# Kernel optimization log

Hardware: AMD Instinct MI355X
Metric: run time of the kernel (lower is better)

The kernel has to match this reference:

```python
import jax, jax.numpy as jnp
import numpy as np

GAMMA = 0.99  # init kwarg


def _discounted_returns(ep_rs):
    # reversed running_add = running_add*gamma + r, emitted per step
    def step(carry, r):
        carry = carry * GAMMA + r
        return carry, carry
    _, out = jax.lax.scan(step, jnp.float32(0.0), ep_rs, reverse=True)
    return out  # [T]


def setup_inputs() -> dict:
    key = jax.random.key(0)
    k1, k2, k3 = jax.random.split(key, 3)
    T, A = 2097152, 18
    weight = jax.random.normal(k1, (T, A), dtype=jnp.float32)
    ep_rs = jax.random.normal(k2, (T,), dtype=jnp.float32)
    ep_as = jax.random.randint(k3, (T,), 0, A, dtype=jnp.int64)
    return {"weight": weight, "ep_rs": ep_rs, "ep_as": ep_as}


def reference(weight, ep_rs, ep_as):
    d = _discounted_returns(ep_rs)
    d = d - jnp.mean(d)
    # cross_entropy with reduction='none': -log_softmax(weight)[t, ep_as[t]]
    logp = jax.nn.log_softmax(weight, axis=-1)  # [T, A]
    neg_log_prob = -jnp.take_along_axis(logp, ep_as[:, None], axis=-1)[:, 0]  # [T]
    return jnp.mean(neg_log_prob * d)
```

## Files before the change

kernel.cpp:

```cpp
#include <hip/hip_runtime.h>
#include <math.h>

#define T_TOTAL 2097152
#define A_DIM   18
#define GAMMA_D 0.99

#define CHUNK 256
#define NC    (T_TOTAL / CHUNK)
#define KTR   14
#define NB_MAIN 4096

__global__ void k_local(const float* __restrict__ r, double* __restrict__ L) {
    const int tid  = blockIdx.x * blockDim.x + threadIdx.x;
    const int c    = tid >> 6;
    const int lane = tid & 63;
    const float4 v = ((const float4*)r)[(size_t)c * 64 + lane];
    const double g = GAMMA_D;
    double w = pow(g, (double)(4 * lane)) *
               ((double)v.x + g * ((double)v.y + g * ((double)v.z + g * (double)v.w)));
    #pragma unroll
    for (int off = 32; off > 0; off >>= 1) w += __shfl_down(w, off, 64);
    if (lane == 0) L[c] = w;
}

__global__ __launch_bounds__(256)
void k_d(const float* __restrict__ r, const double* __restrict__ L,
         double* __restrict__ d) {
    const int tid = threadIdx.x, lane = tid & 63, wv = tid >> 6;
    const int c = blockIdx.x * 4 + wv;
    const double g  = GAMMA_D;
    const double G_ = pow(g, 256.0);
    double acc = 0.0, wG = 1.0;
    #pragma unroll
    for (int m = 0; m < KTR; ++m) {
        const int idx = c + 1 + m;
        if (idx < NC) acc += wG * L[idx];
        wG *= G_;
    }
    const float4 v = ((const float4*)r)[(size_t)c * 64 + lane];
    const double u3 = (double)v.w;
    const double u2 = (double)v.z + g * u3;
    const double u1 = (double)v.y + g * u2;
    const double u0 = (double)v.x + g * u1;
    const double w4 = pow(g, (double)(4 * lane));
    double S = w4 * u0;
    #pragma unroll
    for (int off = 1; off < 64; off <<= 1) {
        const double t = __shfl_down(S, off, 64);
        S += (lane + off < 64) ? t : 0.0;
    }
    double Snext = __shfl_down(S, 1, 64);
    if (lane == 63) Snext = 0.0;
    const double A  = (1.0 / w4) * (Snext + G_ * acc);
    const double ig = 1.0 / g;
    const double d0 = u0 + A;
    const double d1 = u1 + ig * A;
    const double d2 = u2 + (ig * ig) * A;
    const double d3 = u3 + (ig * ig * ig) * A;
    double2* dp = (double2*)(d + (size_t)c * CHUNK + 4 * lane);
    dp[0] = make_double2(d0, d1);
    dp[1] = make_double2(d2, d3);
}

__global__ __launch_bounds__(256, 4)
void k_main(const float* __restrict__ wgt, const int* __restrict__ act,
            const double* __restrict__ dret, double* __restrict__ partials) {
    __shared__ double red[12];
    const int tid  = threadIdx.x;
    const int lane = tid & 63, wv = tid >> 6;
    const size_t t0 = ((size_t)blockIdx.x * 256 + tid) * 2;

    const float4* wp = (const float4*)(wgt + t0 * A_DIM);
    float w[36];
    #pragma unroll
    for (int q = 0; q < 9; ++q) {
        const float4 v = wp[q];
        w[4*q+0] = v.x; w[4*q+1] = v.y; w[4*q+2] = v.z; w[4*q+3] = v.w;
    }
    const int2    aa = *(const int2*)(act + t0);
    const double2 dd = *(const double2*)(dret + t0);

    double s_n = 0.0, s_nd = 0.0;
    double s_d = dd.x + dd.y;
    {
        float mx = w[0];
        #pragma unroll
        for (int j = 1; j < A_DIM; ++j) mx = fmaxf(mx, w[j]);
        float s = 0.0f, wsel = 0.0f;
        #pragma unroll
        for (int j = 0; j < A_DIM; ++j) {
            s += expf(w[j] - mx);
            wsel = (j == aa.x) ? w[j] : wsel;
        }
        const float nlp = mx + logf(s) - wsel;
        s_n += (double)nlp;  s_nd += (double)nlp * dd.x;
    }
    {
        float mx = w[18];
        #pragma unroll
        for (int j = 1; j < A_DIM; ++j) mx = fmaxf(mx, w[18 + j]);
        float s = 0.0f, wsel = 0.0f;
        #pragma unroll
        for (int j = 0; j < A_DIM; ++j) {
            s += expf(w[18 + j] - mx);
            wsel = (j == aa.y) ? w[18 + j] : wsel;
        }
        const float nlp = mx + logf(s) - wsel;
        s_n += (double)nlp;  s_nd += (double)nlp * dd.y;
    }

    #pragma unroll
    for (int off = 32; off > 0; off >>= 1) {
        s_d  += __shfl_down(s_d,  off, 64);
        s_n  += __shfl_down(s_n,  off, 64);
        s_nd += __shfl_down(s_nd, off, 64);
    }
    if (lane == 0) { red[wv*3+0] = s_d; red[wv*3+1] = s_n; red[wv*3+2] = s_nd; }
    __syncthreads();
    if (tid == 0) {
        double a = 0.0, b = 0.0, cc = 0.0;
        #pragma unroll
        for (int q = 0; q < 4; ++q) { a += red[q*3]; b += red[q*3+1]; cc += red[q*3+2]; }
        partials[blockIdx.x*3+0] = a;
        partials[blockIdx.x*3+1] = b;
        partials[blockIdx.x*3+2] = cc;
    }
}

__global__ void k_final(const double* __restrict__ partials, float* __restrict__ out) {
    __shared__ double red[12];
    const int tid = threadIdx.x;
    double a = 0.0, b = 0.0, c = 0.0;
    for (int i = tid; i < NB_MAIN; i += 256) {
        a += partials[i*3+0];
        b += partials[i*3+1];
        c += partials[i*3+2];
    }
    #pragma unroll
    for (int off = 32; off > 0; off >>= 1) {
        a += __shfl_down(a, off, 64);
        b += __shfl_down(b, off, 64);
        c += __shfl_down(c, off, 64);
    }
    const int lane = tid & 63, wv = tid >> 6;
    if (lane == 0) { red[wv*3+0] = a; red[wv*3+1] = b; red[wv*3+2] = c; }
    __syncthreads();
    if (tid == 0) {
        double A_ = 0.0, B_ = 0.0, C_ = 0.0;
        #pragma unroll
        for (int i = 0; i < 4; ++i) { A_ += red[i*3]; B_ += red[i*3+1]; C_ += red[i*3+2]; }
        const double invT = 1.0 / (double)T_TOTAL;
        out[0] = (float)((C_ - (A_ * invT) * B_) * invT);
    }
}

extern "C" void kernel_launch(void* const* d_in, const int* in_sizes, int n_in,
                              void* d_out, int out_size, void* d_ws, size_t ws_size,
                              hipStream_t stream) {
    const float* weight = (const float*)d_in[0];
    const float* ep_rs  = (const float*)d_in[1];
    const int*   ep_as  = (const int*)  d_in[2];
    float* out = (float*)d_out;

    char* ws = (char*)d_ws;
    double* L        = (double*)(ws);
    double* dret     = (double*)(ws + (1 << 16));
    double* partials = (double*)(ws + (1 << 16) + (16 << 20));

    k_local <<<T_TOTAL / 4 / 256, 256, 0, stream>>>(ep_rs, L);
    k_d     <<<NC / 4,            256, 0, stream>>>(ep_rs, L, dret);
    k_main  <<<NB_MAIN,           256, 0, stream>>>(weight, ep_as, dret, partials);
    k_final <<<1,                 256, 0, stream>>>(partials, out);
}
```

Measured before the change: 240.3 us.

## Fuse discounted-return scan into softmax kernel with chunk-local lookahead in LDS

Merges the three kernels (chunk-sum, discounted-return scan, log-softmax reduction) into one kernel. Each block covers 4 chunks and recomputes the weighted sums of the next 17 chunks it needs for the truncated lookahead, writing the returns to LDS instead of a 16 MB global buffer. The weight loads for the first half are issued before the scan so they overlap it. This removes two launches and the global write and reread of the returns, at the cost of extra reads of ep_rs and more LDS and register use per block.

```diff
diff --git a/kernel.cpp b/kernel.cpp
--- a/kernel.cpp
+++ b/kernel.cpp
@@ -8,92 +8,98 @@
 #define CHUNK 256
 #define NC    (T_TOTAL / CHUNK)
 #define KTR   14
-#define NB_MAIN 4096
-
-__global__ void k_local(const float* __restrict__ r, double* __restrict__ L) {
-    const int tid  = blockIdx.x * blockDim.x + threadIdx.x;
-    const int c    = tid >> 6;
-    const int lane = tid & 63;
-    const float4 v = ((const float4*)r)[(size_t)c * 64 + lane];
-    const double g = GAMMA_D;
-    double w = pow(g, (double)(4 * lane)) *
-               ((double)v.x + g * ((double)v.y + g * ((double)v.z + g * (double)v.w)));
-    #pragma unroll
-    for (int off = 32; off > 0; off >>= 1) w += __shfl_down(w, off, 64);
-    if (lane == 0) L[c] = w;
-}
-
-__global__ __launch_bounds__(256)
-void k_d(const float* __restrict__ r, const double* __restrict__ L,
-         double* __restrict__ d) {
-    const int tid = threadIdx.x, lane = tid & 63, wv = tid >> 6;
-    const int c = blockIdx.x * 4 + wv;
-    const double g  = GAMMA_D;
-    const double G_ = pow(g, 256.0);
-    double acc = 0.0, wG = 1.0;
-    #pragma unroll
-    for (int m = 0; m < KTR; ++m) {
-        const int idx = c + 1 + m;
-        if (idx < NC) acc += wG * L[idx];
-        wG *= G_;
-    }
-    const float4 v = ((const float4*)r)[(size_t)c * 64 + lane];
-    const double u3 = (double)v.w;
-    const double u2 = (double)v.z + g * u3;
-    const double u1 = (double)v.y + g * u2;
-    const double u0 = (double)v.x + g * u1;
-    const double w4 = pow(g, (double)(4 * lane));
-    double S = w4 * u0;
-    #pragma unroll
-    for (int off = 1; off < 64; off <<= 1) {
-        const double t = __shfl_down(S, off, 64);
-        S += (lane + off < 64) ? t : 0.0;
-    }
-    double Snext = __shfl_down(S, 1, 64);
-    if (lane == 63) Snext = 0.0;
-    const double A  = (1.0 / w4) * (Snext + G_ * acc);
-    const double ig = 1.0 / g;
-    const double d0 = u0 + A;
-    const double d1 = u1 + ig * A;
-    const double d2 = u2 + (ig * ig) * A;
-    const double d3 = u3 + (ig * ig * ig) * A;
-    double2* dp = (double2*)(d + (size_t)c * CHUNK + 4 * lane);
-    dp[0] = make_double2(d0, d1);
-    dp[1] = make_double2(d2, d3);
-}
+#define CPB   4
+#define NB    (NC / CPB)
 
 __global__ __launch_bounds__(256, 4)
-void k_main(const float* __restrict__ wgt, const int* __restrict__ act,
-            const double* __restrict__ dret, double* __restrict__ partials) {
+void k_mega(const float* __restrict__ wgt, const int* __restrict__ act,
+            const float* __restrict__ r, double* __restrict__ partials) {
+    __shared__ double ldsL[17];
+    __shared__ double ldsD[CPB * CHUNK];
     __shared__ double red[12];
     const int tid  = threadIdx.x;
     const int lane = tid & 63, wv = tid >> 6;
-    const size_t t0 = ((size_t)blockIdx.x * 256 + tid) * 2;
+    const int c0   = blockIdx.x * CPB;
+    const double g  = GAMMA_D;
+    const double G_ = pow(g, 256.0);
+    const double w4 = pow(g, (double)(4 * lane));
 
-    const float4* wp = (const float4*)(wgt + t0 * A_DIM);
+    const size_t rowBase = (size_t)c0 * CHUNK;
+    const float4* wp0 = (const float4*)(wgt + (rowBase + 2 * (size_t)tid) * A_DIM);
+    float4 a0[9];
+    #pragma unroll
+    for (int q = 0; q < 9; ++q) a0[q] = wp0[q];
+    const int2 aa0 = *(const int2*)(act + rowBase + 2 * tid);
+
+    #pragma unroll
+    for (int i = 0; i < 5; ++i) {
+        const int k  = wv + 4 * i;
+        const int cc = c0 + 1 + k;
+        if (k < 17) {
+            double val = 0.0;
+            if (cc < NC) {
+                const float4 v = ((const float4*)r)[(size_t)cc * 64 + lane];
+                val = w4 * ((double)v.x + g * ((double)v.y + g * ((double)v.z + g * (double)v.w)));
+                #pragma unroll
+                for (int off = 32; off > 0; off >>= 1) val += __shfl_down(val, off, 64);
+            }
+            if (lane == 0) ldsL[k] = val;
+        }
+    }
+    __syncthreads();
+
+    {
+        double acc = 0.0, wG = 1.0;
+        #pragma unroll
+        for (int m = 0; m < KTR; ++m) { acc += wG * ldsL[wv + m]; wG *= G_; }
+        const int c = c0 + wv;
+        const float4 v = ((const float4*)r)[(size_t)c * 64 + lane];
+        const double u3 = (double)v.w;
+        const double u2 = (double)v.z + g * u3;
+        const double u1 = (double)v.y + g * u2;
+        const double u0 = (double)v.x + g * u1;
+        double S = w4 * u0;
+        #pragma unroll
+        for (int off = 1; off < 64; off <<= 1) {
+            const double t = __shfl_down(S, off, 64);
+            S += (lane + off < 64) ? t : 0.0;
+        }
+        double Snext = __shfl_down(S, 1, 64);
+        if (lane == 63) Snext = 0.0;
+        const double A  = (1.0 / w4) * (Snext + G_ * acc);
+        const double ig = 1.0 / g;
+        double* dp = ldsD + wv * CHUNK + 4 * lane;
+        dp[0] = u0 + A;
+        dp[1] = u1 + ig * A;
+        dp[2] = u2 + (ig * ig) * A;
+        dp[3] = u3 + (ig * ig * ig) * A;
+    }
+    __syncthreads();
+
+    const float4* wp1 = (const float4*)(wgt + (rowBase + 512 + 2 * (size_t)tid) * A_DIM);
+    float4 a1[9];
+    #pragma unroll
+    for (int q = 0; q < 9; ++q) a1[q] = wp1[q];
+    const int2    aa1 = *(const int2*)(act + rowBase + 512 + 2 * tid);
+    const double2 dd0 = *(const double2*)(ldsD + 2 * tid);
+    const double2 dd1 = *(const double2*)(ldsD + 512 + 2 * tid);
+
+    double s_n = 0.0, s_nd = 0.0;
+    double s_d = dd0.x + dd0.y + dd1.x + dd1.y;
     float w[36];
     #pragma unroll
     for (int q = 0; q < 9; ++q) {
-        const float4 v = wp[q];
-        w[4*q+0] = v.x; w[4*q+1] = v.y; w[4*q+2] = v.z; w[4*q+3] = v.w;
+        w[4*q+0] = a0[q].x; w[4*q+1] = a0[q].y; w[4*q+2] = a0[q].z; w[4*q+3] = a0[q].w;
     }
-    const int2    aa = *(const int2*)(act + t0);
-    const double2 dd = *(const double2*)(dret + t0);
-
-    double s_n = 0.0, s_nd = 0.0;
-    double s_d = dd.x + dd.y;
     {
         float mx = w[0];
         #pragma unroll
         for (int j = 1; j < A_DIM; ++j) mx = fmaxf(mx, w[j]);
         float s = 0.0f, wsel = 0.0f;
         #pragma unroll
-        for (int j = 0; j < A_DIM; ++j) {
-            s += expf(w[j] - mx);
-            wsel = (j == aa.x) ? w[j] : wsel;
-        }
+        for (int j = 0; j < A_DIM; ++j) { s += expf(w[j] - mx); wsel = (j == aa0.x) ? w[j] : wsel; }
         const float nlp = mx + logf(s) - wsel;
-        s_n += (double)nlp;  s_nd += (double)nlp * dd.x;
+        s_n += (double)nlp;  s_nd += (double)nlp * dd0.x;
     }
     {
         float mx = w[18];
@@ -101,12 +107,33 @@
         for (int j = 1; j < A_DIM; ++j) mx = fmaxf(mx, w[18 + j]);
         float s = 0.0f, wsel = 0.0f;
         #pragma unroll
-        for (int j = 0; j < A_DIM; ++j) {
-            s += expf(w[18 + j] - mx);
-            wsel = (j == aa.y) ? w[18 + j] : wsel;
-        }
+        for (int j = 0; j < A_DIM; ++j) { s += expf(w[18 + j] - mx); wsel = (j == aa0.y) ? w[18 + j] : wsel; }
         const float nlp = mx + logf(s) - wsel;
-        s_n += (double)nlp;  s_nd += (double)nlp * dd.y;
+        s_n += (double)nlp;  s_nd += (double)nlp * dd0.y;
+    }
+    #pragma unroll
+    for (int q = 0; q < 9; ++q) {
+        w[4*q+0] = a1[q].x; w[4*q+1] = a1[q].y; w[4*q+2] = a1[q].z; w[4*q+3] = a1[q].w;
+    }
+    {
+        float mx = w[0];
+        #pragma unroll
+        for (int j = 1; j < A_DIM; ++j) mx = fmaxf(mx, w[j]);
+        float s = 0.0f, wsel = 0.0f;
+        #pragma unroll
+        for (int j = 0; j < A_DIM; ++j) { s += expf(w[j] - mx); wsel = (j == aa1.x) ? w[j] : wsel; }
+        const float nlp = mx + logf(s) - wsel;
+        s_n += (double)nlp;  s_nd += (double)nlp * dd1.x;
+    }
+    {
+        float mx = w[18];
+        #pragma unroll
+        for (int j = 1; j < A_DIM; ++j) mx = fmaxf(mx, w[18 + j]);
+        float s = 0.0f, wsel = 0.0f;
+        #pragma unroll
+        for (int j = 0; j < A_DIM; ++j) { s += expf(w[18 + j] - mx); wsel = (j == aa1.y) ? w[18 + j] : wsel; }
+        const float nlp = mx + logf(s) - wsel;
+        s_n += (double)nlp;  s_nd += (double)nlp * dd1.y;
     }
 
     #pragma unroll
@@ -131,7 +158,7 @@
     __shared__ double red[12];
     const int tid = threadIdx.x;
     double a = 0.0, b = 0.0, c = 0.0;
-    for (int i = tid; i < NB_MAIN; i += 256) {
+    for (int i = tid; i < NB; i += 256) {
         a += partials[i*3+0];
         b += partials[i*3+1];
         c += partials[i*3+2];
@@ -162,13 +189,8 @@
     const int*   ep_as  = (const int*)  d_in[2];
     float* out = (float*)d_out;
 
-    char* ws = (char*)d_ws;
-    double* L        = (double*)(ws);
-    double* dret     = (double*)(ws + (1 << 16));
-    double* partials = (double*)(ws + (1 << 16) + (16 << 20));
+    double* partials = (double*)d_ws;
 
-    k_local <<<T_TOTAL / 4 / 256, 256, 0, stream>>>(ep_rs, L);
-    k_d     <<<NC / 4,            256, 0, stream>>>(ep_rs, L, dret);
-    k_main  <<<NB_MAIN,           256, 0, stream>>>(weight, ep_as, dret, partials);
-    k_final <<<1,                 256, 0, stream>>>(partials, out);
+    k_mega  <<<NB, 256, 0, stream>>>(weight, ep_as, ep_rs, partials);
+    k_final <<<1,  256, 0, stream>>>(partials, out);
 }
```

New measurement: 232.6 us. 3.2% less time.

## Fuse discounted-return scan, log-softmax and reduction into one kernel

Applied to the files above, without the earlier changes.

Replaces the four-kernel pipeline with a single kernel. Each block recomputes the chunk-local discounted sums it needs for its own chunk and the 14-chunk lookahead, builds the returns in LDS instead of a 16 MB global buffer, and consumes them directly in the cross-entropy reduction. The final reduction uses double atomics plus a last-block flag instead of a separate kernel, with a memset to reset the accumulators. This removes the global round trip for the returns and the extra launches, at the cost of redundant reads of the reward vector and atomic contention on three doubles.

```diff
diff --git a/kernel.cpp b/kernel.cpp
--- a/kernel.cpp
+++ b/kernel.cpp
@@ -8,90 +8,96 @@
 #define CHUNK 256
 #define NC    (T_TOTAL / CHUNK)
 #define KTR   14
-#define NB_MAIN 4096
+#define CPB   4
+#define NB    (NC / CPB)
+#define BLK   512
 
-__global__ void k_local(const float* __restrict__ r, double* __restrict__ L) {
-    const int tid  = blockIdx.x * blockDim.x + threadIdx.x;
-    const int c    = tid >> 6;
-    const int lane = tid & 63;
-    const float4 v = ((const float4*)r)[(size_t)c * 64 + lane];
-    const double g = GAMMA_D;
-    double w = pow(g, (double)(4 * lane)) *
-               ((double)v.x + g * ((double)v.y + g * ((double)v.z + g * (double)v.w)));
-    #pragma unroll
-    for (int off = 32; off > 0; off >>= 1) w += __shfl_down(w, off, 64);
-    if (lane == 0) L[c] = w;
-}
-
-__global__ __launch_bounds__(256)
-void k_d(const float* __restrict__ r, const double* __restrict__ L,
-         double* __restrict__ d) {
-    const int tid = threadIdx.x, lane = tid & 63, wv = tid >> 6;
-    const int c = blockIdx.x * 4 + wv;
+__global__ __launch_bounds__(BLK, 4)
+void k_mega(const float* __restrict__ wgt, const int* __restrict__ act,
+            const float* __restrict__ r, double* __restrict__ acc,
+            unsigned int* __restrict__ flag, float* __restrict__ out) {
+    __shared__ double ldsL[17];
+    __shared__ double ldsD[CPB * CHUNK];
+    __shared__ double red[24];
+    const int tid  = threadIdx.x;
+    const int lane = tid & 63, wv = tid >> 6;
+    const int c0   = blockIdx.x * CPB;
     const double g  = GAMMA_D;
     const double G_ = pow(g, 256.0);
-    double acc = 0.0, wG = 1.0;
+    const double w4 = pow(g, (double)(4 * lane));
+
+    const int cc0 = c0 + 1 + wv;
+    const int cc1 = c0 + 1 + wv + 8;
+    const int cc2 = c0 + 1 + wv + 16;
+    float4 rv0 = (cc0 < NC) ? ((const float4*)r)[(size_t)cc0 * 64 + lane] : make_float4(0,0,0,0);
+    float4 rv1 = (cc1 < NC) ? ((const float4*)r)[(size_t)cc1 * 64 + lane] : make_float4(0,0,0,0);
+    float4 rv2 = (wv == 0 && cc2 < NC) ? ((const float4*)r)[(size_t)cc2 * 64 + lane] : make_float4(0,0,0,0);
+    float4 rown = (wv < CPB) ? ((const float4*)r)[(size_t)(c0 + wv) * 64 + lane] : make_float4(0,0,0,0);
+
+    const size_t rowBase = (size_t)blockIdx.x * (CPB * CHUNK);
+    const float4* wp = (const float4*)(wgt + (rowBase + 2 * (size_t)tid) * A_DIM);
+    float4 a[9];
     #pragma unroll
-    for (int m = 0; m < KTR; ++m) {
-        const int idx = c + 1 + m;
-        if (idx < NC) acc += wG * L[idx];
-        wG *= G_;
+    for (int q = 0; q < 9; ++q) a[q] = wp[q];
+    const int2 aa = *(const int2*)(act + rowBase + 2 * tid);
+
+    double vs0 = w4 * ((double)rv0.x + g * ((double)rv0.y + g * ((double)rv0.z + g * (double)rv0.w)));
+    double vs1 = w4 * ((double)rv1.x + g * ((double)rv1.y + g * ((double)rv1.z + g * (double)rv1.w)));
+    double vs2 = w4 * ((double)rv2.x + g * ((double)rv2.y + g * ((double)rv2.z + g * (double)rv2.w)));
+    #pragma unroll
+    for (int off = 32; off > 0; off >>= 1) {
+        vs0 += __shfl_down(vs0, off, 64);
+        vs1 += __shfl_down(vs1, off, 64);
+        vs2 += __shfl_down(vs2, off, 64);
     }
-    const float4 v = ((const float4*)r)[(size_t)c * 64 + lane];
-    const double u3 = (double)v.w;
-    const double u2 = (double)v.z + g * u3;
-    const double u1 = (double)v.y + g * u2;
-    const double u0 = (double)v.x + g * u1;
-    const double w4 = pow(g, (double)(4 * lane));
-    double S = w4 * u0;
-    #pragma unroll
-    for (int off = 1; off < 64; off <<= 1) {
-        const double t = __shfl_down(S, off, 64);
-        S += (lane + off < 64) ? t : 0.0;
+    if (lane == 0) {
+        ldsL[wv]     = vs0;
+        ldsL[wv + 8] = vs1;
+        if (wv == 0) ldsL[16] = vs2;
     }
-    double Snext = __shfl_down(S, 1, 64);
-    if (lane == 63) Snext = 0.0;
-    const double A  = (1.0 / w4) * (Snext + G_ * acc);
-    const double ig = 1.0 / g;
-    const double d0 = u0 + A;
-    const double d1 = u1 + ig * A;
-    const double d2 = u2 + (ig * ig) * A;
-    const double d3 = u3 + (ig * ig * ig) * A;
-    double2* dp = (double2*)(d + (size_t)c * CHUNK + 4 * lane);
-    dp[0] = make_double2(d0, d1);
-    dp[1] = make_double2(d2, d3);
-}
+    __syncthreads();
 
-__global__ __launch_bounds__(256, 4)
-void k_main(const float* __restrict__ wgt, const int* __restrict__ act,
-            const double* __restrict__ dret, double* __restrict__ partials) {
-    __shared__ double red[12];
-    const int tid  = threadIdx.x;
-    const int lane = tid & 63, wv = tid >> 6;
-    const size_t t0 = ((size_t)blockIdx.x * 256 + tid) * 2;
+    if (wv < CPB) {
+        double acc_c = 0.0, wG = 1.0;
+        #pragma unroll
+        for (int m = 0; m < KTR; ++m) { acc_c += wG * ldsL[wv + m]; wG *= G_; }
+        const double u3 = (double)rown.w;
+        const double u2 = (double)rown.z + g * u3;
+        const double u1 = (double)rown.y + g * u2;
+        const double u0 = (double)rown.x + g * u1;
+        double S = w4 * u0;
+        #pragma unroll
+        for (int off = 1; off < 64; off <<= 1) {
+            const double t = __shfl_down(S, off, 64);
+            S += (lane + off < 64) ? t : 0.0;
+        }
+        double Snext = __shfl_down(S, 1, 64);
+        if (lane == 63) Snext = 0.0;
+        const double A  = (1.0 / w4) * (Snext + G_ * acc_c);
+        const double ig = 1.0 / g;
+        double* dp = ldsD + wv * CHUNK + 4 * lane;
+        dp[0] = u0 + A;
+        dp[1] = u1 + ig * A;
+        dp[2] = u2 + (ig * ig) * A;
+        dp[3] = u3 + (ig * ig * ig) * A;
+    }
+    __syncthreads();
 
-    const float4* wp = (const float4*)(wgt + t0 * A_DIM);
+    const double2 dd = *(const double2*)(ldsD + 2 * tid);
+    double s_n = 0.0, s_nd = 0.0;
+    double s_d = dd.x + dd.y;
     float w[36];
     #pragma unroll
     for (int q = 0; q < 9; ++q) {
-        const float4 v = wp[q];
-        w[4*q+0] = v.x; w[4*q+1] = v.y; w[4*q+2] = v.z; w[4*q+3] = v.w;
+        w[4*q+0] = a[q].x; w[4*q+1] = a[q].y; w[4*q+2] = a[q].z; w[4*q+3] = a[q].w;
     }
-    const int2    aa = *(const int2*)(act + t0);
-    const double2 dd = *(const double2*)(dret + t0);
-
-    double s_n = 0.0, s_nd = 0.0;
-    double s_d = dd.x + dd.y;
     {
         float mx = w[0];
         #pragma unroll
         for (int j = 1; j < A_DIM; ++j) mx = fmaxf(mx, w[j]);
         float s = 0.0f, wsel = 0.0f;
         #pragma unroll
-        for (int j = 0; j < A_DIM; ++j) {
-            s += expf(w[j] - mx);
-            wsel = (j == aa.x) ? w[j] : wsel;
-        }
+        for (int j = 0; j < A_DIM; ++j) { s += expf(w[j] - mx); wsel = (j == aa.x) ? w[j] : wsel; }
         const float nlp = mx + logf(s) - wsel;
         s_n += (double)nlp;  s_nd += (double)nlp * dd.x;
     }
@@ -101,10 +107,7 @@
         for (int j = 1; j < A_DIM; ++j) mx = fmaxf(mx, w[18 + j]);
         float s = 0.0f, wsel = 0.0f;
         #pragma unroll
-        for (int j = 0; j < A_DIM; ++j) {
-            s += expf(w[18 + j] - mx);
-            wsel = (j == aa.y) ? w[18 + j] : wsel;
-        }
+        for (int j = 0; j < A_DIM; ++j) { s += expf(w[18 + j] - mx); wsel = (j == aa.y) ? w[18 + j] : wsel; }
         const float nlp = mx + logf(s) - wsel;
         s_n += (double)nlp;  s_nd += (double)nlp * dd.y;
     }
@@ -118,39 +121,22 @@
     if (lane == 0) { red[wv*3+0] = s_d; red[wv*3+1] = s_n; red[wv*3+2] = s_nd; }
     __syncthreads();
     if (tid == 0) {
-        double a = 0.0, b = 0.0, cc = 0.0;
+        double pa = 0.0, pb = 0.0, pc = 0.0;
         #pragma unroll
-        for (int q = 0; q < 4; ++q) { a += red[q*3]; b += red[q*3+1]; cc += red[q*3+2]; }
-        partials[blockIdx.x*3+0] = a;
-        partials[blockIdx.x*3+1] = b;
-        partials[blockIdx.x*3+2] = cc;
-    }
-}
-
-__global__ void k_final(const double* __restrict__ partials, float* __restrict__ out) {
-    __shared__ double red[12];
-    const int tid = threadIdx.x;
-    double a = 0.0, b = 0.0, c = 0.0;
-    for (int i = tid; i < NB_MAIN; i += 256) {
-        a += partials[i*3+0];
-        b += partials[i*3+1];
-        c += partials[i*3+2];
-    }
-    #pragma unroll
-    for (int off = 32; off > 0; off >>= 1) {
-        a += __shfl_down(a, off, 64);
-        b += __shfl_down(b, off, 64);
-        c += __shfl_down(c, off, 64);
-    }
-    const int lane = tid & 63, wv = tid >> 6;
-    if (lane == 0) { red[wv*3+0] = a; red[wv*3+1] = b; red[wv*3+2] = c; }
-    __syncthreads();
-    if (tid == 0) {
-        double A_ = 0.0, B_ = 0.0, C_ = 0.0;
-        #pragma unroll
-        for (int i = 0; i < 4; ++i) { A_ += red[i*3]; B_ += red[i*3+1]; C_ += red[i*3+2]; }
-        const double invT = 1.0 / (double)T_TOTAL;
-        out[0] = (float)((C_ - (A_ * invT) * B_) * invT);
+        for (int q = 0; q < 8; ++q) { pa += red[q*3]; pb += red[q*3+1]; pc += red[q*3+2]; }
+        atomicAdd(&acc[0], pa);
+        atomicAdd(&acc[1], pb);
+        atomicAdd(&acc[2], pc);
+        __threadfence();
+        const unsigned int old = atomicAdd(flag, 1u);
+        if (old == NB - 1) {
+            __threadfence();
+            const double sd  = atomicAdd(&acc[0], 0.0);
+            const double sn  = atomicAdd(&acc[1], 0.0);
+            const double snd = atomicAdd(&acc[2], 0.0);
+            const double invT = 1.0 / (double)T_TOTAL;
+            out[0] = (float)((snd - (sd * invT) * sn) * invT);
+        }
     }
 }
 
@@ -162,13 +148,9 @@
     const int*   ep_as  = (const int*)  d_in[2];
     float* out = (float*)d_out;
 
-    char* ws = (char*)d_ws;
-    double* L        = (double*)(ws);
-    double* dret     = (double*)(ws + (1 << 16));
-    double* partials = (double*)(ws + (1 << 16) + (16 << 20));
+    double*       acc  = (double*)d_ws;
+    unsigned int* flag = (unsigned int*)((char*)d_ws + 24);
 
-    k_local <<<T_TOTAL / 4 / 256, 256, 0, stream>>>(ep_rs, L);
-    k_d     <<<NC / 4,            256, 0, stream>>>(ep_rs, L, dret);
-    k_main  <<<NB_MAIN,           256, 0, stream>>>(weight, ep_as, dret, partials);
-    k_final <<<1,                 256, 0, stream>>>(partials, out);
+    hipMemsetAsync(d_ws, 0, 64, stream);
+    k_mega<<<NB, BLK, 0, stream>>>(weight, ep_as, ep_rs, acc, flag, out);
 }
```

After: 319.2 us. +32.8%, slower.
